# Performance work log

Hardware: AMD Instinct MI355X
Metric: run time of the kernel (lower is better)

Reference implementation:

```python
import jax, jax.numpy as jnp
import numpy as np

HEADS = 8
DIM_HEAD = 64
SCALE = DIM_HEAD ** (-0.5)


def setup_inputs() -> dict:
    key = jax.random.key(0)
    k1, k2, k3 = jax.random.split(key, 3)
    b, l, c = 8, 4096, 512
    x = jax.random.normal(k1, (b, l, c), dtype=jnp.float32)
    w_qkv = jax.random.normal(k2, (3 * c, c), dtype=jnp.float32) * (c ** -0.5)
    w_out = jax.random.normal(k3, (c, c), dtype=jnp.float32) * (c ** -0.5)
    b_out = jnp.zeros((c,), dtype=jnp.float32)
    return {"x": x, "w_qkv": w_qkv, "w_out": w_out, "b_out": b_out}


def reference(x, w_qkv, w_out, b_out):
    b, l, c = x.shape
    h = HEADS
    lh = l // h
    # to_qkv: Linear(dim, 3*dim, bias=False)
    qkv = x @ w_qkv.T                                   # (b, l, 3c)
    qkv = qkv.reshape(b, lh, h, 3, c).transpose(3, 0, 2, 1, 4)  # (3, b, h, l/h, c)
    q, k, v = qkv[0], qkv[1], qkv[2]                    # each (b, h, l/h, c)
    # transpose(-2,-1): attention is over the CHANNEL axis
    q = jnp.swapaxes(q, -2, -1)                         # (b, h, c, l/h)
    k = jnp.swapaxes(k, -2, -1)                         # (b, h, c, l/h)
    v = jnp.swapaxes(v, -2, -1)                         # (b, h, c, l/h)
    attn = jnp.einsum('bhcl,bhdl->bhcd', q, k) * SCALE  # (b, h, c, c)
    attn = jax.nn.softmax(attn, axis=-1)
    y = jnp.einsum('bhcd,bhdl->bhcl', attn, v)          # (b, h, c, l/h)
    y = y.transpose(0, 3, 1, 2).reshape(b, l, c)        # (b, l/h, h, c) -> (b, l, c)
    # to_out: Linear(dim, dim) + Dropout (identity at eval)
    out = y @ w_out.T + b_out
    return out
```

## Files before the change

kernel.cpp:

```cpp
#include <hip/hip_runtime.h>
#include <stdint.h>
#include <stddef.h>

typedef _Float16 f16;
typedef _Float16 f16x8 __attribute__((ext_vector_type(8)));
typedef _Float16 f16x4 __attribute__((ext_vector_type(4)));
typedef float f32x4 __attribute__((ext_vector_type(4)));

__device__ __forceinline__ void gload16(const void* g, void* l) {
    auto gp = (const __attribute__((address_space(1))) uint32_t*)(uintptr_t)g;
    auto lp = (__attribute__((address_space(3))) uint32_t*)(uintptr_t)l;
    __builtin_amdgcn_global_load_lds(gp, lp, 16, 0, 0);
}

__device__ __forceinline__ f16x4 cvt4(f32x4 v) {
    return f16x4{ (f16)v[0], (f16)v[1], (f16)v[2], (f16)v[3] };
}

__global__ __launch_bounds__(256) void prep_k(const float* __restrict__ x,
                                              const float* __restrict__ wqkv,
                                              const float* __restrict__ wout,
                                              f16* __restrict__ xb,
                                              f16* __restrict__ wqb,
                                              f16* __restrict__ wob) {
    int tid = blockIdx.x * blockDim.x + threadIdx.x;
    int stride = gridDim.x * blockDim.x;
    for (int i = tid; i < 4194304; i += stride) {
        float4 v = ((const float4*)x)[i];
        *(f16x4*)(xb + (size_t)i * 4) = f16x4{ (f16)v.x, (f16)v.y, (f16)v.z, (f16)v.w };
    }
    for (int i = tid; i < 196608; i += stride) {
        float4 v = ((const float4*)wqkv)[i];
        *(f16x4*)(wqb + (size_t)i * 4) = f16x4{ (f16)v.x, (f16)v.y, (f16)v.z, (f16)v.w };
    }
    for (int i = tid; i < 65536; i += stride) {
        float4 v = ((const float4*)wout)[i];
        *(f16x4*)(wob + (size_t)i * 4) = f16x4{ (f16)v.x, (f16)v.y, (f16)v.z, (f16)v.w };
    }
}


#define MFMA_BLK(MH, NH, AF, BF) do {                                           \
    __builtin_amdgcn_s_setprio(1);                                              \
    if (swp) {                                                                  \
        for (int mi = 0; mi < 4; ++mi)                                          \
            for (int ni = 0; ni < 2; ++ni)                                      \
                for (int kk = 0; kk < 2; ++kk)                                  \
                    acc[(MH)*4+mi][(NH)*2+ni] = __builtin_amdgcn_mfma_f32_16x16x32_f16( \
                        BF[ni][kk], AF[mi][kk], acc[(MH)*4+mi][(NH)*2+ni], 0, 0, 0);    \
    } else {                                                                    \
        for (int mi = 0; mi < 4; ++mi)                                          \
            for (int ni = 0; ni < 2; ++ni)                                      \
                for (int kk = 0; kk < 2; ++kk)                                  \
                    acc[(MH)*4+mi][(NH)*2+ni] = __builtin_amdgcn_mfma_f32_16x16x32_f16( \
                        AF[mi][kk], BF[ni][kk], acc[(MH)*4+mi][(NH)*2+ni], 0, 0, 0);    \
    }                                                                           \
    __builtin_amdgcn_s_setprio(0);                                              \
} while (0)

#define STAGE_A(h, li) gload16(srcA[(h)*2+(li)], &lds[nb][0][((h)*128+(li)*64+wid*8)*64])
#define STAGE_B(h, li) gload16(srcB[(h)*2+(li)], &lds[nb][1][((h)*128+(li)*64+wid*8)*64])

template <int MODE>
__global__ __launch_bounds__(512, 2) void g8_k(const f16* __restrict__ A0,
                                               const f16* __restrict__ B0,
                                               void* __restrict__ C0,
                                               void* __restrict__ C1,
                                               void* __restrict__ C2,
                                               const float* __restrict__ bias) {
    __shared__ f16 lds[2][2][16384];

    const int tid = threadIdx.x;
    const int lane = tid & 63;
    const int wid = tid >> 6;
    const int wr = wid >> 2;
    const int wc = wid & 3;

    int tm, tn, bh = 0;
    bool qk = false, swp;
    const int bid = blockIdx.x;
    if constexpr (MODE == 0) {
        int swz = (bid & 7) * 96 + (bid >> 3);
        tm = (swz / 6) * 256; tn = (swz % 6) * 256;
        qk = tn < 1024; swp = !qk;
    } else if constexpr (MODE == 1 || MODE == 2) {
        int swz = (bid & 7) * 32 + (bid >> 3);
        bh = swz >> 2; tm = ((swz >> 1) & 1) * 256; tn = (swz & 1) * 256;
        swp = (MODE == 1);
    } else {
        int swz = (bid & 7) * 32 + (bid >> 3);
        tm = (swz >> 1) * 256; tn = (swz & 1) * 256;
        swp = true;
    }

    const size_t bhoff = (MODE == 1 || MODE == 2) ? (size_t)bh * 262144 : 0;
    const f16* At = A0 + bhoff + (size_t)tm * 512;
    const f16* Bt = B0 + bhoff + (size_t)tn * 512;

    const f16* srcA[4];
    const f16* srcB[4];
#pragma unroll
    for (int h = 0; h < 2; ++h)
#pragma unroll
        for (int li = 0; li < 2; ++li) {
            int r = h * 128 + li * 64 + (tid >> 3);
            int c8 = (tid & 7) ^ ((r & 7) ^ ((r >> 3) & 7));
            srcA[h * 2 + li] = At + (size_t)r * 512 + c8 * 8;
            srcB[h * 2 + li] = Bt + (size_t)r * 512 + c8 * 8;
        }

    int aoff[16];
    int boff[8];
#pragma unroll
    for (int mh = 0; mh < 2; ++mh)
#pragma unroll
        for (int mi = 0; mi < 4; ++mi) {
            int r = qk ? (mh * 128 + (lane & 15) * 8 + wr * 4 + mi)
                       : (mh * 128 + wr * 64 + mi * 16 + (lane & 15));
#pragma unroll
            for (int kk = 0; kk < 2; ++kk) {
                int c8 = (lane >> 4) + kk * 4;
                aoff[mh * 8 + mi * 2 + kk] = r * 64 + (c8 ^ ((r & 7) ^ ((r >> 3) & 7))) * 8;
            }
        }
#pragma unroll
    for (int nh = 0; nh < 2; ++nh)
#pragma unroll
        for (int ni = 0; ni < 2; ++ni) {
            int r = nh * 128 + wc * 32 + ni * 16 + (lane & 15);
#pragma unroll
            for (int kk = 0; kk < 2; ++kk) {
                int c8 = (lane >> 4) + kk * 4;
                boff[nh * 4 + ni * 2 + kk] = r * 64 + (c8 ^ ((r & 7) ^ ((r >> 3) & 7))) * 8;
            }
        }

    f32x4 acc[8][4] = {};
    f16x8 afA[4][2], afB[4][2], bf0[2][2], bf1[2][2];

    {
        int nb = 0;
        STAGE_A(0, 0); STAGE_A(0, 1);
        STAGE_B(0, 0); STAGE_B(0, 1);
        STAGE_B(1, 0); STAGE_B(1, 1);
        STAGE_A(1, 0); STAGE_A(1, 1);
#pragma unroll
        for (int i = 0; i < 4; ++i) { srcA[i] += 64; srcB[i] += 64; }
    }
    asm volatile("s_waitcnt vmcnt(4)" ::: "memory");
    __builtin_amdgcn_s_barrier();

#pragma unroll 1
    for (int t = 0; t < 7; ++t) {
        const f16* LA = &lds[t & 1][0][0];
        const f16* LB = &lds[t & 1][1][0];
        const int nb = (t + 1) & 1;

#pragma unroll
        for (int mi = 0; mi < 4; ++mi)
#pragma unroll
            for (int kk = 0; kk < 2; ++kk)
                afA[mi][kk] = *(const f16x8*)(LA + aoff[mi * 2 + kk]);
#pragma unroll
        for (int ni = 0; ni < 2; ++ni)
#pragma unroll
            for (int kk = 0; kk < 2; ++kk)
                bf0[ni][kk] = *(const f16x8*)(LB + boff[ni * 2 + kk]);
        STAGE_A(0, 0); STAGE_A(0, 1); STAGE_B(0, 0); STAGE_B(0, 1);
        asm volatile("s_waitcnt vmcnt(6)" ::: "memory");
        __builtin_amdgcn_s_barrier();
        MFMA_BLK(0, 0, afA, bf0);
        __builtin_amdgcn_s_barrier();

#pragma unroll
        for (int ni = 0; ni < 2; ++ni)
#pragma unroll
            for (int kk = 0; kk < 2; ++kk)
                bf1[ni][kk] = *(const f16x8*)(LB + boff[4 + ni * 2 + kk]);
        STAGE_B(1, 0); STAGE_B(1, 1);
        asm volatile("s_waitcnt vmcnt(6)" ::: "memory");
        __builtin_amdgcn_s_barrier();
        MFMA_BLK(0, 1, afA, bf1);
        __builtin_amdgcn_s_barrier();

#pragma unroll
        for (int mi = 0; mi < 4; ++mi)
#pragma unroll
            for (int kk = 0; kk < 2; ++kk)
                afB[mi][kk] = *(const f16x8*)(LA + aoff[8 + mi * 2 + kk]);
        STAGE_A(1, 0); STAGE_A(1, 1);
        __builtin_amdgcn_s_barrier();
        MFMA_BLK(1, 1, afB, bf1);
        __builtin_amdgcn_s_barrier();

        asm volatile("s_waitcnt vmcnt(4)" ::: "memory");
        __builtin_amdgcn_s_barrier();
        MFMA_BLK(1, 0, afB, bf0);
        __builtin_amdgcn_s_barrier();

#pragma unroll
        for (int i = 0; i < 4; ++i) { srcA[i] += 64; srcB[i] += 64; }
    }

    {
        const f16* LA = &lds[1][0][0];
        const f16* LB = &lds[1][1][0];
#pragma unroll
        for (int mi = 0; mi < 4; ++mi)
#pragma unroll
            for (int kk = 0; kk < 2; ++kk)
                afA[mi][kk] = *(const f16x8*)(LA + aoff[mi * 2 + kk]);
#pragma unroll
        for (int ni = 0; ni < 2; ++ni)
#pragma unroll
            for (int kk = 0; kk < 2; ++kk)
                bf0[ni][kk] = *(const f16x8*)(LB + boff[ni * 2 + kk]);
        asm volatile("s_waitcnt vmcnt(2)" ::: "memory");
        __builtin_amdgcn_s_barrier();
        MFMA_BLK(0, 0, afA, bf0);
        __builtin_amdgcn_s_barrier();

#pragma unroll
        for (int ni = 0; ni < 2; ++ni)
#pragma unroll
            for (int kk = 0; kk < 2; ++kk)
                bf1[ni][kk] = *(const f16x8*)(LB + boff[4 + ni * 2 + kk]);
        asm volatile("s_waitcnt vmcnt(0)" ::: "memory");
        __builtin_amdgcn_s_barrier();
        MFMA_BLK(0, 1, afA, bf1);
        __builtin_amdgcn_s_barrier();

#pragma unroll
        for (int mi = 0; mi < 4; ++mi)
#pragma unroll
            for (int kk = 0; kk < 2; ++kk)
                afB[mi][kk] = *(const f16x8*)(LA + aoff[8 + mi * 2 + kk]);
        __builtin_amdgcn_s_barrier();
        MFMA_BLK(1, 1, afB, bf1);
        MFMA_BLK(1, 0, afB, bf0);
    }

    if constexpr (MODE == 0) {
        const int b = tm >> 12;
        if (qk) {
            f16* dst = (f16*)(tn < 512 ? C0 : C1);
            const int lt = (tm & 4095) >> 3;
            const int cb = (tn & 511) + wc * 32;
#pragma unroll
            for (int mf = 0; mf < 8; ++mf) {
                int h = wr * 4 + (mf & 3);
                int lh0 = lt + (mf >> 2) * 16 + (lane >> 4) * 4;
#pragma unroll
                for (int nf = 0; nf < 4; ++nf) {
                    int c = cb + (nf >> 1) * 128 + (nf & 1) * 16 + (lane & 15);
                    *(f16x4*)(dst + ((size_t)((b * 8 + h) * 512 + c)) * 512 + lh0) =
                        cvt4(acc[mf][nf]);
                }
            }
        } else {
            f16* dst = (f16*)C2;
#pragma unroll
            for (int mf = 0; mf < 8; ++mf) {
                int m = (tm & 4095) + (mf >> 2) * 128 + wr * 64 + (mf & 3) * 16 + (lane & 15);
                int h = m & 7;
                int lh = m >> 3;
#pragma unroll
                for (int nf = 0; nf < 4; ++nf) {
                    int d0 = (tn - 1024) + (nf >> 1) * 128 + wc * 32 + (nf & 1) * 16 + (lane >> 4) * 4;
                    *(f16x4*)(dst + ((size_t)((b * 8 + h) * 512 + lh)) * 512 + d0) =
                        cvt4(acc[mf][nf]);
                }
            }
        }
    } else if constexpr (MODE == 1) {
        float* S = (float*)C0 + (size_t)bh * 262144;
#pragma unroll
        for (int mf = 0; mf < 8; ++mf) {
            int cm = tm + (mf >> 2) * 128 + wr * 64 + (mf & 3) * 16 + (lane & 15);
#pragma unroll
            for (int nf = 0; nf < 4; ++nf) {
                int d0 = tn + (nf >> 1) * 128 + wc * 32 + (nf & 1) * 16 + (lane >> 4) * 4;
                *(f32x4*)(S + (size_t)cm * 512 + d0) = acc[mf][nf] * 0.125f;
            }
        }
    } else if constexpr (MODE == 2) {
        f16* yb = (f16*)C0;
        const int b = bh >> 3, h = bh & 7;
#pragma unroll
        for (int mf = 0; mf < 8; ++mf) {
            int c0 = tm + (mf >> 2) * 128 + wr * 64 + (mf & 3) * 16 + (lane >> 4) * 4;
#pragma unroll
            for (int nf = 0; nf < 4; ++nf) {
                int l = tn + (nf >> 1) * 128 + wc * 32 + (nf & 1) * 16 + (lane & 15);
                size_t tok = (size_t)b * 4096 + (size_t)l * 8 + h;
                *(f16x4*)(yb + tok * 512 + c0) = cvt4(acc[mf][nf]);
            }
        }
    } else {
        float* O = (float*)C0;
#pragma unroll
        for (int mf = 0; mf < 8; ++mf) {
            int m = tm + (mf >> 2) * 128 + wr * 64 + (mf & 3) * 16 + (lane & 15);
#pragma unroll
            for (int nf = 0; nf < 4; ++nf) {
                int n0 = tn + (nf >> 1) * 128 + wc * 32 + (nf & 1) * 16 + (lane >> 4) * 4;
                float4 bv = *(const float4*)(bias + n0);
                f32x4 v = acc[mf][nf];
                v[0] += bv.x; v[1] += bv.y; v[2] += bv.z; v[3] += bv.w;
                *(f32x4*)(O + (size_t)m * 512 + n0) = v;
            }
        }
    }
}

__global__ __launch_bounds__(256) void softmax_k(const float* __restrict__ S,
                                                 f16* __restrict__ P) {
    int row = blockIdx.x * 4 + (threadIdx.x >> 6);
    int lane = threadIdx.x & 63;
    const float* src = S + (size_t)row * 512 + lane * 8;
    float v[8];
    *(float4*)&v[0] = *(const float4*)src;
    *(float4*)&v[4] = *(const float4*)(src + 4);
    float m = v[0];
#pragma unroll
    for (int i = 1; i < 8; ++i) m = fmaxf(m, v[i]);
#pragma unroll
    for (int off = 1; off < 64; off <<= 1) m = fmaxf(m, __shfl_xor(m, off, 64));
    float s = 0.f, e[8];
#pragma unroll
    for (int i = 0; i < 8; ++i) { e[i] = __expf(v[i] - m); s += e[i]; }
#pragma unroll
    for (int off = 1; off < 64; off <<= 1) s += __shfl_xor(s, off, 64);
    float inv = 1.0f / s;
    f16x8 pk;
#pragma unroll
    for (int i = 0; i < 8; ++i) pk[i] = (f16)(e[i] * inv);
    *(f16x8*)(P + (size_t)row * 512 + lane * 8) = pk;
}

extern "C" void kernel_launch(void* const* d_in, const int* in_sizes, int n_in,
                              void* d_out, int out_size, void* d_ws, size_t ws_size,
                              hipStream_t stream) {
    const float* x = (const float*)d_in[0];
    const float* wqkv = (const float*)d_in[1];
    const float* wout = (const float*)d_in[2];
    const float* bout = (const float*)d_in[3];
    float* out = (float*)d_out;
    char* ws = (char*)d_ws;
    const size_t MBs = 1u << 20;

    f16* xb  = (f16*)(ws + 0);
    f16* wqb = (f16*)(ws + 32 * MBs);
    f16* wob = (f16*)(ws + 34 * MBs);
    f16* Qb  = (f16*)(ws + 35 * MBs);
    f16* Kb  = (f16*)(ws + 67 * MBs);
    f16* Vb  = (f16*)(ws + 99 * MBs);
    float* Sb = (float*)(ws + 131 * MBs);
    f16* Pb  = xb;
    f16* yb  = Qb;

    prep_k<<<1024, 256, 0, stream>>>(x, wqkv, wout, xb, wqb, wob);
    g8_k<0><<<768, 512, 0, stream>>>(xb, wqb, Qb, Kb, Vb, nullptr);
    g8_k<1><<<256, 512, 0, stream>>>(Qb, Kb, Sb, nullptr, nullptr, nullptr);
    softmax_k<<<8192, 256, 0, stream>>>(Sb, Pb);
    g8_k<2><<<256, 512, 0, stream>>>(Pb, Vb, yb, nullptr, nullptr, nullptr);
    g8_k<3><<<256, 512, 0, stream>>>(yb, wob, out, nullptr, nullptr, bout);
}
```

Baseline: 208.3 us.

## Restructure GEMM main loop with full-tile prefetch and store scores in fp16

Rewrites the g8_k K-loop as an unrolled TILE macro. Each tile issues all global-to-LDS loads for the next buffer up front, drops most per-quadrant barriers to a single wait+barrier per tile, and preloads the next tile's A/B fragments during the last MFMA quadrant. MFMA ordering is changed to put kk outermost. Separately, the attention score matrix S is written and read as fp16 instead of fp32, which halves the bytes moved between the QK^T GEMM and softmax at some cost in precision of the pre-softmax logits.

Result: slower. 421.0 us (+102.1%).

```diff
diff --git a/kernel.cpp b/kernel.cpp
--- a/kernel.cpp
+++ b/kernel.cpp
@@ -40,26 +40,61 @@
 }
 
 
-#define MFMA_BLK(MH, NH, AF, BF) do {                                           \
+#define MFMA_Q(MH, NH, AF, BF) do {                                             \
     __builtin_amdgcn_s_setprio(1);                                              \
     if (swp) {                                                                  \
-        for (int mi = 0; mi < 4; ++mi)                                          \
-            for (int ni = 0; ni < 2; ++ni)                                      \
-                for (int kk = 0; kk < 2; ++kk)                                  \
-                    acc[(MH)*4+mi][(NH)*2+ni] = __builtin_amdgcn_mfma_f32_16x16x32_f16( \
-                        BF[ni][kk], AF[mi][kk], acc[(MH)*4+mi][(NH)*2+ni], 0, 0, 0);    \
+        _Pragma("unroll") for (int kk = 0; kk < 2; ++kk)                        \
+        _Pragma("unroll") for (int mi = 0; mi < 4; ++mi)                        \
+        _Pragma("unroll") for (int ni = 0; ni < 2; ++ni)                        \
+            acc[(MH)*4+mi][(NH)*2+ni] = __builtin_amdgcn_mfma_f32_16x16x32_f16( \
+                BF[ni][kk], AF[mi][kk], acc[(MH)*4+mi][(NH)*2+ni], 0, 0, 0);    \
     } else {                                                                    \
-        for (int mi = 0; mi < 4; ++mi)                                          \
-            for (int ni = 0; ni < 2; ++ni)                                      \
-                for (int kk = 0; kk < 2; ++kk)                                  \
-                    acc[(MH)*4+mi][(NH)*2+ni] = __builtin_amdgcn_mfma_f32_16x16x32_f16( \
-                        AF[mi][kk], BF[ni][kk], acc[(MH)*4+mi][(NH)*2+ni], 0, 0, 0);    \
+        _Pragma("unroll") for (int kk = 0; kk < 2; ++kk)                        \
+        _Pragma("unroll") for (int mi = 0; mi < 4; ++mi)                        \
+        _Pragma("unroll") for (int ni = 0; ni < 2; ++ni)                        \
+            acc[(MH)*4+mi][(NH)*2+ni] = __builtin_amdgcn_mfma_f32_16x16x32_f16( \
+                AF[mi][kk], BF[ni][kk], acc[(MH)*4+mi][(NH)*2+ni], 0, 0, 0);    \
     }                                                                           \
     __builtin_amdgcn_s_setprio(0);                                              \
 } while (0)
 
-#define STAGE_A(h, li) gload16(srcA[(h)*2+(li)], &lds[nb][0][((h)*128+(li)*64+wid*8)*64])
-#define STAGE_B(h, li) gload16(srcB[(h)*2+(li)], &lds[nb][1][((h)*128+(li)*64+wid*8)*64])
+#define RD_AFA(LA) do { _Pragma("unroll") for (int mi = 0; mi < 4; ++mi)        \
+    _Pragma("unroll") for (int kk = 0; kk < 2; ++kk)                            \
+        afA[mi][kk] = *(const f16x8*)((LA) + aoff[mi * 2 + kk]); } while (0)
+#define RD_AFB(LA) do { _Pragma("unroll") for (int mi = 0; mi < 4; ++mi)        \
+    _Pragma("unroll") for (int kk = 0; kk < 2; ++kk)                            \
+        afB[mi][kk] = *(const f16x8*)((LA) + aoff[8 + mi * 2 + kk]); } while (0)
+#define RD_BF0(LB) do { _Pragma("unroll") for (int ni = 0; ni < 2; ++ni)        \
+    _Pragma("unroll") for (int kk = 0; kk < 2; ++kk)                            \
+        bf0[ni][kk] = *(const f16x8*)((LB) + boff[ni * 2 + kk]); } while (0)
+#define RD_BF1(LB) do { _Pragma("unroll") for (int ni = 0; ni < 2; ++ni)        \
+    _Pragma("unroll") for (int kk = 0; kk < 2; ++kk)                            \
+        bf1[ni][kk] = *(const f16x8*)((LB) + boff[4 + ni * 2 + kk]); } while (0)
+
+#define STAGE_A(h, li, NB) gload16(srcA[(h)*2+(li)], &lds[NB][0][((h)*128+(li)*64+wid*8)*64])
+#define STAGE_B(h, li, NB) gload16(srcB[(h)*2+(li)], &lds[NB][1][((h)*128+(li)*64+wid*8)*64])
+#define STAGE_ALL(NB) do {                                                      \
+    STAGE_A(0,0,NB); STAGE_A(0,1,NB); STAGE_B(0,0,NB); STAGE_B(0,1,NB);         \
+    STAGE_B(1,0,NB); STAGE_B(1,1,NB); STAGE_A(1,0,NB); STAGE_A(1,1,NB); } while (0)
+
+#define TILE(CB, NB, STG, FINAL) do {                                           \
+    RD_BF1(&lds[CB][1][0]);                                                     \
+    if (STG) STAGE_ALL(NB);                                                     \
+    MFMA_Q(0, 0, afA, bf0);                                                     \
+    RD_AFB(&lds[CB][0][0]);                                                     \
+    MFMA_Q(0, 1, afA, bf1);                                                     \
+    MFMA_Q(1, 1, afB, bf1);                                                     \
+    if (!FINAL) {                                                               \
+        asm volatile("s_waitcnt vmcnt(0)" ::: "memory");                        \
+        __builtin_amdgcn_s_barrier();                                           \
+        RD_AFA(&lds[NB][0][0]);                                                 \
+    }                                                                           \
+    MFMA_Q(1, 0, afB, bf0);                                                     \
+    if (!FINAL) {                                                               \
+        RD_BF0(&lds[NB][1][0]);                                                 \
+        _Pragma("unroll") for (int z = 0; z < 4; ++z) { srcA[z] += 64; srcB[z] += 64; } \
+    }                                                                           \
+} while (0)
 
 template <int MODE>
 __global__ __launch_bounds__(512, 2) void g8_k(const f16* __restrict__ A0,
@@ -138,107 +173,21 @@
     f32x4 acc[8][4] = {};
     f16x8 afA[4][2], afB[4][2], bf0[2][2], bf1[2][2];
 
-    {
-        int nb = 0;
-        STAGE_A(0, 0); STAGE_A(0, 1);
-        STAGE_B(0, 0); STAGE_B(0, 1);
-        STAGE_B(1, 0); STAGE_B(1, 1);
-        STAGE_A(1, 0); STAGE_A(1, 1);
-#pragma unroll
-        for (int i = 0; i < 4; ++i) { srcA[i] += 64; srcB[i] += 64; }
-    }
-    asm volatile("s_waitcnt vmcnt(4)" ::: "memory");
+    STAGE_ALL(0);
+#pragma unroll
+    for (int z = 0; z < 4; ++z) { srcA[z] += 64; srcB[z] += 64; }
+    asm volatile("s_waitcnt vmcnt(0)" ::: "memory");
     __builtin_amdgcn_s_barrier();
+    RD_AFA(&lds[0][0][0]);
+    RD_BF0(&lds[0][1][0]);
 
 #pragma unroll 1
-    for (int t = 0; t < 7; ++t) {
-        const f16* LA = &lds[t & 1][0][0];
-        const f16* LB = &lds[t & 1][1][0];
-        const int nb = (t + 1) & 1;
-
-#pragma unroll
-        for (int mi = 0; mi < 4; ++mi)
-#pragma unroll
-            for (int kk = 0; kk < 2; ++kk)
-                afA[mi][kk] = *(const f16x8*)(LA + aoff[mi * 2 + kk]);
-#pragma unroll
-        for (int ni = 0; ni < 2; ++ni)
-#pragma unroll
-            for (int kk = 0; kk < 2; ++kk)
-                bf0[ni][kk] = *(const f16x8*)(LB + boff[ni * 2 + kk]);
-        STAGE_A(0, 0); STAGE_A(0, 1); STAGE_B(0, 0); STAGE_B(0, 1);
-        asm volatile("s_waitcnt vmcnt(6)" ::: "memory");
-        __builtin_amdgcn_s_barrier();
-        MFMA_BLK(0, 0, afA, bf0);
-        __builtin_amdgcn_s_barrier();
-
-#pragma unroll
-        for (int ni = 0; ni < 2; ++ni)
-#pragma unroll
-            for (int kk = 0; kk < 2; ++kk)
-                bf1[ni][kk] = *(const f16x8*)(LB + boff[4 + ni * 2 + kk]);
-        STAGE_B(1, 0); STAGE_B(1, 1);
-        asm volatile("s_waitcnt vmcnt(6)" ::: "memory");
-        __builtin_amdgcn_s_barrier();
-        MFMA_BLK(0, 1, afA, bf1);
-        __builtin_amdgcn_s_barrier();
-
-#pragma unroll
-        for (int mi = 0; mi < 4; ++mi)
-#pragma unroll
-            for (int kk = 0; kk < 2; ++kk)
-                afB[mi][kk] = *(const f16x8*)(LA + aoff[8 + mi * 2 + kk]);
-        STAGE_A(1, 0); STAGE_A(1, 1);
-        __builtin_amdgcn_s_barrier();
-        MFMA_BLK(1, 1, afB, bf1);
-        __builtin_amdgcn_s_barrier();
-
-        asm volatile("s_waitcnt vmcnt(4)" ::: "memory");
-        __builtin_amdgcn_s_barrier();
-        MFMA_BLK(1, 0, afB, bf0);
-        __builtin_amdgcn_s_barrier();
-
-#pragma unroll
-        for (int i = 0; i < 4; ++i) { srcA[i] += 64; srcB[i] += 64; }
-    }
-
-    {
-        const f16* LA = &lds[1][0][0];
-        const f16* LB = &lds[1][1][0];
-#pragma unroll
-        for (int mi = 0; mi < 4; ++mi)
-#pragma unroll
-            for (int kk = 0; kk < 2; ++kk)
-                afA[mi][kk] = *(const f16x8*)(LA + aoff[mi * 2 + kk]);
-#pragma unroll
-        for (int ni = 0; ni < 2; ++ni)
-#pragma unroll
-            for (int kk = 0; kk < 2; ++kk)
-                bf0[ni][kk] = *(const f16x8*)(LB + boff[ni * 2 + kk]);
-        asm volatile("s_waitcnt vmcnt(2)" ::: "memory");
-        __builtin_amdgcn_s_barrier();
-        MFMA_BLK(0, 0, afA, bf0);
-        __builtin_amdgcn_s_barrier();
-
-#pragma unroll
-        for (int ni = 0; ni < 2; ++ni)
-#pragma unroll
-            for (int kk = 0; kk < 2; ++kk)
-                bf1[ni][kk] = *(const f16x8*)(LB + boff[4 + ni * 2 + kk]);
-        asm volatile("s_waitcnt vmcnt(0)" ::: "memory");
-        __builtin_amdgcn_s_barrier();
-        MFMA_BLK(0, 1, afA, bf1);
-        __builtin_amdgcn_s_barrier();
-
-#pragma unroll
-        for (int mi = 0; mi < 4; ++mi)
-#pragma unroll
-            for (int kk = 0; kk < 2; ++kk)
-                afB[mi][kk] = *(const f16x8*)(LA + aoff[8 + mi * 2 + kk]);
-        __builtin_amdgcn_s_barrier();
-        MFMA_BLK(1, 1, afB, bf1);
-        MFMA_BLK(1, 0, afB, bf0);
-    }
+    for (int i = 0; i < 3; ++i) {
+        TILE(0, 1, true, false);
+        TILE(1, 0, true, false);
+    }
+    TILE(0, 1, true, false);
+    TILE(1, 0, false, true);
 
     if constexpr (MODE == 0) {
         const int b = tm >> 12;
@@ -273,14 +222,14 @@
             }
         }
     } else if constexpr (MODE == 1) {
-        float* S = (float*)C0 + (size_t)bh * 262144;
+        f16* S = (f16*)C0 + (size_t)bh * 262144;
 #pragma unroll
         for (int mf = 0; mf < 8; ++mf) {
             int cm = tm + (mf >> 2) * 128 + wr * 64 + (mf & 3) * 16 + (lane & 15);
 #pragma unroll
             for (int nf = 0; nf < 4; ++nf) {
                 int d0 = tn + (nf >> 1) * 128 + wc * 32 + (nf & 1) * 16 + (lane >> 4) * 4;
-                *(f32x4*)(S + (size_t)cm * 512 + d0) = acc[mf][nf] * 0.125f;
+                *(f16x4*)(S + (size_t)cm * 512 + d0) = cvt4(acc[mf][nf] * 0.125f);
             }
         }
     } else if constexpr (MODE == 2) {
@@ -313,22 +262,22 @@
     }
 }
 
-__global__ __launch_bounds__(256) void softmax_k(const float* __restrict__ S,
+__global__ __launch_bounds__(256) void softmax_k(const f16* __restrict__ S,
                                                  f16* __restrict__ P) {
     int row = blockIdx.x * 4 + (threadIdx.x >> 6);
     int lane = threadIdx.x & 63;
-    const float* src = S + (size_t)row * 512 + lane * 8;
-    float v[8];
-    *(float4*)&v[0] = *(const float4*)src;
-    *(float4*)&v[4] = *(const float4*)(src + 4);
-    float m = v[0];
-#pragma unroll
-    for (int i = 1; i < 8; ++i) m = fmaxf(m, v[i]);
+    f16x8 v = *(const f16x8*)(S + (size_t)row * 512 + lane * 8);
+    float f[8];
+#pragma unroll
+    for (int i = 0; i < 8; ++i) f[i] = (float)v[i];
+    float m = f[0];
+#pragma unroll
+    for (int i = 1; i < 8; ++i) m = fmaxf(m, f[i]);
 #pragma unroll
     for (int off = 1; off < 64; off <<= 1) m = fmaxf(m, __shfl_xor(m, off, 64));
     float s = 0.f, e[8];
 #pragma unroll
-    for (int i = 0; i < 8; ++i) { e[i] = __expf(v[i] - m); s += e[i]; }
+    for (int i = 0; i < 8; ++i) { e[i] = __expf(f[i] - m); s += e[i]; }
 #pragma unroll
     for (int off = 1; off < 64; off <<= 1) s += __shfl_xor(s, off, 64);
     float inv = 1.0f / s;
@@ -355,7 +304,7 @@
     f16* Qb  = (f16*)(ws + 35 * MBs);
     f16* Kb  = (f16*)(ws + 67 * MBs);
     f16* Vb  = (f16*)(ws + 99 * MBs);
-    float* Sb = (float*)(ws + 131 * MBs);
+    f16* Sb  = (f16*)(ws + 131 * MBs);
     f16* Pb  = xb;
     f16* yb  = Qb;
 
```
